# Kernel optimization log

Hardware: AMD Instinct MI355X
Metric: run time of the kernel (lower is better)

The kernel has to match this reference:

```python
import jax, jax.numpy as jnp
import numpy as np

MAX_INT8 = 127.5  # maxtext KVQuant MAX_INT8
AR_ORDER = (1, 2, 0, 3)  # ar_cache_axis_order: logical (B,S,H,D) -> stored (S,H,B,D)

B, H, D = 4, 16, 128
S_AR = 4096 - 1024  # max_target_length - max_prefill_length


def setup_inputs() -> dict:
    key = jax.random.key(0)
    ks = jax.random.split(key, 6)
    return {
        # new decode-step key/value, logical layout (B, 1, H, D)
        "key": jax.random.normal(ks[0], (B, 1, H, D), jnp.float32),
        "value": jax.random.normal(ks[1], (B, 1, H, D), jnp.float32),
        # existing AR cache in stored layout (S, H, B, D); holds int8-valued floats
        "cached_ar_key": jnp.rint(jax.random.normal(ks[2], (S_AR, H, B, D), jnp.float32) * 40.0),
        "cached_ar_value": jnp.rint(jax.random.normal(ks[3], (S_AR, H, B, D), jnp.float32) * 40.0),
        # per-(b,s,h) scales, stored layout (S, H, B, 1); strictly positive
        "cached_ar_key_scale": jax.random.uniform(ks[4], (S_AR, H, B, 1), jnp.float32, 0.5, 1.5),
        "cached_ar_value_scale": jax.random.uniform(ks[5], (S_AR, H, B, 1), jnp.float32, 0.5, 1.5),
        "ar_cache_index": 1234,
    }


def _quantize_dkv(kv):
    # KVQuant.quantize with axis_cfg='dkv': max |kv| over CACHE_KV axis, keepdims
    scale = jnp.max(jnp.abs(kv), axis=-1, keepdims=True)
    qvalue = jnp.rint(kv * (MAX_INT8 / scale))  # int8-valued (kept float for parity)
    return qvalue, scale


def reference(key, value, cached_ar_key, cached_ar_value,
              cached_ar_key_scale, cached_ar_value_scale, ar_cache_index):
    # 1) inline per-axis quantization of the new K/V step
    qk, k_scale = _quantize_dkv(key)      # (B,1,H,D), (B,1,H,1)
    qv, v_scale = _quantize_dkv(value)

    # 2) transpose to stored cache layout (S,H,B,D)
    t = lambda x: jnp.transpose(x, AR_ORDER)
    idx4 = (ar_cache_index, 0, 0, 0)

    # 3) dynamic-slice scatter-append at the current sequence position
    new_k = jax.lax.dynamic_update_slice(cached_ar_key, t(qk), idx4)
    new_v = jax.lax.dynamic_update_slice(cached_ar_value, t(qv), idx4)
    new_k_scale = jax.lax.dynamic_update_slice(cached_ar_key_scale, t(k_scale), idx4)
    new_v_scale = jax.lax.dynamic_update_slice(cached_ar_value_scale, t(v_scale), idx4)

    # 4) dequantized full cache as consumed by attention: q * scale / MAX_INT8
    k_deq = new_k * (new_k_scale * (1.0 / MAX_INT8))
    v_deq = new_v * (new_v_scale * (1.0 / MAX_INT8))
    return (k_deq, v_deq)
```

## Files before the change

kernel.cpp:

```cpp
#include <hip/hip_runtime.h>

#define S_AR 3072
#define NH 16
#define NB 4
#define ND 128
#define NTOT (S_AR * NH * NB * ND)
#define N4   (NTOT / 4)

__device__ __forceinline__ float inv_max_int8() { return 1.0f / 127.5f; }

__global__ void __launch_bounds__(256) dequant_stream(
    const float4* __restrict__ ck, const float4* __restrict__ cv,
    const float*  __restrict__ ksc, const float* __restrict__ vsc,
    float4* __restrict__ ok, float4* __restrict__ ov)
{
    const float inv = inv_max_int8();
    int stride = gridDim.x * blockDim.x;
    for (int i = blockIdx.x * blockDim.x + threadIdx.x; i < N4; i += stride) {
        int row = i >> 5;
        float ks = ksc[row] * inv;
        float vs = vsc[row] * inv;
        float4 k = ck[i];
        float4 v = cv[i];
        k.x *= ks; k.y *= ks; k.z *= ks; k.w *= ks;
        v.x *= vs; v.y *= vs; v.z *= vs; v.w *= vs;
        ok[i] = k;
        ov[i] = v;
    }
}

__global__ void __launch_bounds__(64) write_new_row(
    const float* __restrict__ key, const float* __restrict__ value,
    const int* __restrict__ idxp, float* __restrict__ out_k, float* __restrict__ out_v)
{
    int g  = blockIdx.x;
    int kv = g & 1;
    int bh = g >> 1;
    int b  = bh / NH;
    int h  = bh % NH;

    const float* src = (kv ? value : key) + (b * NH + h) * ND;
    int lane = threadIdx.x;
    float x0 = src[lane];
    float x1 = src[lane + 64];

    float m = fmaxf(fabsf(x0), fabsf(x1));
    #pragma unroll
    for (int off = 32; off; off >>= 1)
        m = fmaxf(m, __shfl_xor(m, off));

    float qs = 127.5f / m;
    float ds = m * inv_max_int8();

    int idx = *idxp;
    float* dst = (kv ? out_v : out_k) + (((size_t)idx * NH + h) * NB + b) * ND;
    dst[lane]      = rintf(x0 * qs) * ds;
    dst[lane + 64] = rintf(x1 * qs) * ds;
}

extern "C" void kernel_launch(void* const* d_in, const int* in_sizes, int n_in,
                              void* d_out, int out_size, void* d_ws, size_t ws_size,
                              hipStream_t stream) {
    const float* key   = (const float*)d_in[0];
    const float* value = (const float*)d_in[1];
    const float* ck    = (const float*)d_in[2];
    const float* cv    = (const float*)d_in[3];
    const float* ksc   = (const float*)d_in[4];
    const float* vsc   = (const float*)d_in[5];
    const int*   idxp  = (const int*)d_in[6];

    float* out_k = (float*)d_out;
    float* out_v = (float*)d_out + NTOT;

    dim3 block(256);
    dim3 grid(2048);
    dequant_stream<<<grid, block, 0, stream>>>(
        (const float4*)ck, (const float4*)cv, ksc, vsc,
        (float4*)out_k, (float4*)out_v);

    write_new_row<<<dim3(128), dim3(64), 0, stream>>>(key, value, idxp, out_k, out_v);
}
```

Baseline: 84.41 us.

## Fuse new-row quantization into streaming dequant kernel with nontemporal accesses

Merges the separate new-row quantize/write kernel into the main dequant streaming kernel, so the row at the current cache index is computed in place and is neither loaded from the old cache nor written twice. Adds nontemporal loads and stores for the streamed cache data and fully unrolls the grid-stride loop using a compile-time iteration count. This removes one kernel launch and the redundant traffic for the updated row. In exchange it adds a branch inside the hot loop and assumes the element count divides evenly by the grid stride.

```diff
diff --git a/kernel.cpp b/kernel.cpp
--- a/kernel.cpp
+++ b/kernel.cpp
@@ -6,56 +6,63 @@
 #define ND 128
 #define NTOT (S_AR * NH * NB * ND)
 #define N4   (NTOT / 4)
+#define TPB 256
+#define BLOCKS 2048
+#define STRIDE (BLOCKS * TPB)
+#define ITERS (N4 / STRIDE)
 
-__device__ __forceinline__ float inv_max_int8() { return 1.0f / 127.5f; }
+typedef float vf4 __attribute__((ext_vector_type(4)));
 
-__global__ void __launch_bounds__(256) dequant_stream(
-    const float4* __restrict__ ck, const float4* __restrict__ cv,
-    const float*  __restrict__ ksc, const float* __restrict__ vsc,
-    float4* __restrict__ ok, float4* __restrict__ ov)
-{
-    const float inv = inv_max_int8();
-    int stride = gridDim.x * blockDim.x;
-    for (int i = blockIdx.x * blockDim.x + threadIdx.x; i < N4; i += stride) {
-        int row = i >> 5;
-        float ks = ksc[row] * inv;
-        float vs = vsc[row] * inv;
-        float4 k = ck[i];
-        float4 v = cv[i];
-        k.x *= ks; k.y *= ks; k.z *= ks; k.w *= ks;
-        v.x *= vs; v.y *= vs; v.z *= vs; v.w *= vs;
-        ok[i] = k;
-        ov[i] = v;
-    }
+__device__ __forceinline__ float max4abs(vf4 a) {
+    return fmaxf(fmaxf(fabsf(a.x), fabsf(a.y)), fmaxf(fabsf(a.z), fabsf(a.w)));
 }
 
-__global__ void __launch_bounds__(64) write_new_row(
-    const float* __restrict__ key, const float* __restrict__ value,
-    const int* __restrict__ idxp, float* __restrict__ out_k, float* __restrict__ out_v)
+__global__ void __launch_bounds__(TPB) kv_dequant_fused(
+    const vf4* __restrict__ key4, const vf4* __restrict__ val4,
+    const vf4* __restrict__ ck,   const vf4* __restrict__ cv,
+    const float* __restrict__ ksc, const float* __restrict__ vsc,
+    const int* __restrict__ idxp,
+    vf4* __restrict__ ok, vf4* __restrict__ ov)
 {
-    int g  = blockIdx.x;
-    int kv = g & 1;
-    int bh = g >> 1;
-    int b  = bh / NH;
-    int h  = bh % NH;
+    const float inv = 1.0f / 127.5f;
+    const int idx = *idxp;
+    const int tid = blockIdx.x * TPB + threadIdx.x;
 
-    const float* src = (kv ? value : key) + (b * NH + h) * ND;
-    int lane = threadIdx.x;
-    float x0 = src[lane];
-    float x1 = src[lane + 64];
-
-    float m = fmaxf(fabsf(x0), fabsf(x1));
     #pragma unroll
-    for (int off = 32; off; off >>= 1)
-        m = fmaxf(m, __shfl_xor(m, off));
-
-    float qs = 127.5f / m;
-    float ds = m * inv_max_int8();
-
-    int idx = *idxp;
-    float* dst = (kv ? out_v : out_k) + (((size_t)idx * NH + h) * NB + b) * ND;
-    dst[lane]      = rintf(x0 * qs) * ds;
-    dst[lane + 64] = rintf(x1 * qs) * ds;
+    for (int it = 0; it < ITERS; ++it) {
+        const int i   = tid + it * STRIDE;
+        const int row = i >> 5;
+        vf4 k, v;
+        if ((row >> 6) != idx) {
+            const float ks = ksc[row] * inv;
+            const float vs = vsc[row] * inv;
+            k = __builtin_nontemporal_load(&ck[i]);
+            v = __builtin_nontemporal_load(&cv[i]);
+            k *= ks;
+            v *= vs;
+        } else {
+            const int h = (row >> 2) & 15;
+            const int b = row & 3;
+            const int off = (b * NH + h) * (ND / 4) + (i & 31);
+            const vf4 kn = key4[off];
+            const vf4 vn = val4[off];
+            float mk = max4abs(kn);
+            float mv = max4abs(vn);
+            #pragma unroll
+            for (int o = 16; o; o >>= 1) {
+                mk = fmaxf(mk, __shfl_xor(mk, o));
+                mv = fmaxf(mv, __shfl_xor(mv, o));
+            }
+            const float qk = 127.5f / mk, dk = mk * inv;
+            const float qv = 127.5f / mv, dv = mv * inv;
+            k.x = rintf(kn.x * qk) * dk; k.y = rintf(kn.y * qk) * dk;
+            k.z = rintf(kn.z * qk) * dk; k.w = rintf(kn.w * qk) * dk;
+            v.x = rintf(vn.x * qv) * dv; v.y = rintf(vn.y * qv) * dv;
+            v.z = rintf(vn.z * qv) * dv; v.w = rintf(vn.w * qv) * dv;
+        }
+        __builtin_nontemporal_store(k, &ok[i]);
+        __builtin_nontemporal_store(v, &ov[i]);
+    }
 }
 
 extern "C" void kernel_launch(void* const* d_in, const int* in_sizes, int n_in,
@@ -72,11 +79,9 @@
     float* out_k = (float*)d_out;
     float* out_v = (float*)d_out + NTOT;
 
-    dim3 block(256);
-    dim3 grid(2048);
-    dequant_stream<<<grid, block, 0, stream>>>(
-        (const float4*)ck, (const float4*)cv, ksc, vsc,
-        (float4*)out_k, (float4*)out_v);
-
-    write_new_row<<<dim3(128), dim3(64), 0, stream>>>(key, value, idxp, out_k, out_v);
+    kv_dequant_fused<<<dim3(BLOCKS), dim3(TPB), 0, stream>>>(
+        (const vf4*)key, (const vf4*)value,
+        (const vf4*)ck, (const vf4*)cv,
+        ksc, vsc, idxp,
+        (vf4*)out_k, (vf4*)out_v);
 }
```

Measured after the change: 76.45 us. 9.4% less time.
